# Kernel optimization log

Measured on AMD Instinct MI355X. Metric: run time of the kernel, lower is better.

Reference implementation:

```python
import jax, jax.numpy as jnp
import numpy as np

N_NODES = 50000
N_EDGES = 1000000
D_IN_V = 64
D_IN_A = 64
D_OUT_V = 64
D_OUT_A = 64


def setup_inputs() -> dict:
    key = jax.random.key(0)
    ks = jax.random.split(key, 12)
    s = 1.0 / np.sqrt(D_IN_V)
    sa = 1.0 / np.sqrt(D_IN_A)
    return {
        "x_v": jax.random.normal(ks[0], (N_NODES, D_IN_V), jnp.float32),
        "x_a": jax.random.normal(ks[1], (N_EDGES, D_IN_A), jnp.float32),
        "arc_index": jax.random.randint(ks[2], (2, N_EDGES), 0, N_NODES, jnp.int32),
        # torch.nn.Linear convention: weight [out, in], y = x @ W.T + b
        "W_vv": jax.random.uniform(ks[3], (D_OUT_V, D_IN_V), jnp.float32, -s, s),
        "b_vv": jax.random.uniform(ks[4], (D_OUT_V,), jnp.float32, -s, s),
        "W_va": jax.random.uniform(ks[5], (D_OUT_V, D_IN_A), jnp.float32, -sa, sa),
        "W_att": jax.random.uniform(ks[6], (1, D_IN_A), jnp.float32, -sa, sa),
        "b_att": jax.random.uniform(ks[7], (1,), jnp.float32, -sa, sa),
        "W_aa": jax.random.uniform(ks[8], (D_OUT_A, D_IN_A), jnp.float32, -sa, sa),
        "b_aa": jax.random.uniform(ks[9], (D_OUT_A,), jnp.float32, -sa, sa),
        "W_av": jax.random.uniform(ks[10], (D_OUT_A, D_IN_V), jnp.float32, -s, s),
    }


def reference(x_v, x_a, arc_index, W_vv, b_vv, W_va, W_att, b_att, W_aa, b_aa, W_av):
    src = arc_index[0]
    dst = arc_index[1]
    num_nodes = x_v.shape[0]

    # h_self = dense_vv(x_v)
    h_self = x_v @ W_vv.T + b_vv                      # [N, out_v]

    # per-edge attention logit e = attention_va(x_a).squeeze(-1)
    e = (x_a @ W_att.T + b_att)[:, 0]                 # [E]

    # segment softmax over incoming edges of each dst node (numerically stable)
    max_per_dst = jax.ops.segment_max(e, dst, num_segments=num_nodes)  # -inf for empty segments
    exp_e = jnp.exp(e - max_per_dst[dst])             # [E]
    denom = jax.ops.segment_sum(exp_e, dst, num_segments=num_nodes)
    attn = exp_e / denom[dst]                         # [E]

    # message = dense_va(x_a) * attn, scatter-add into dst
    msg = (x_a @ W_va.T) * attn[:, None]              # [E, out_v]
    h_msg = jax.ops.segment_sum(msg, dst, num_segments=num_nodes)
    h_v = h_msg + h_self

    # arc update: dense_aa(x_a) + dense_av(x_v[src]) + dense_av(x_v[dst])
    h_a = x_a @ W_aa.T + b_aa + x_v[src] @ W_av.T + x_v[dst] @ W_av.T
    return (h_v, h_a)
```

## Files before the change

### kernel.cpp

```cpp
#include <hip/hip_runtime.h>

#define NE 1000000
#define NN 50000
#define D 64

__global__ __launch_bounds__(256) void k_init(float4* __restrict__ acc4,
                                              float* __restrict__ denom){
  int i = blockIdx.x*256 + threadIdx.x;
  if (i < NN*D/4) acc4[i] = make_float4(0.f,0.f,0.f,0.f);
  if (i < NN)     denom[i] = 0.f;
}

__global__ __launch_bounds__(256) void k_node(const float* __restrict__ x_v,
    const float* __restrict__ W_vv, const float* __restrict__ b_vv,
    const float* __restrict__ W_av, float* __restrict__ h_v,
    float* __restrict__ p_av){
  __shared__ float4 xrow[4][2][16];
  int lane = threadIdx.x & 63;
  int wv   = threadIdx.x >> 6;
  int wid  = __builtin_amdgcn_readfirstlane(blockIdx.x*4 + wv);
  int nw   = gridDim.x*4;
  float4 wvv[16], wav[16];
  #pragma unroll
  for (int q = 0; q < 16; q++){
    wvv[q] = *(const float4*)(W_vv + lane*D + q*4);
    wav[q] = *(const float4*)(W_av + lane*D + q*4);
  }
  float bv = b_vv[lane];
  int p = 0;
  for (int n = wid; n < NN; n += nw, p ^= 1){
    float xv = x_v[(size_t)n*D + lane];
    ((float*)xrow[wv][p])[lane] = xv;
    float a0=0.f,a1=0.f,b0=0.f,b1=0.f;
    #pragma unroll
    for (int q = 0; q < 16; q++){
      float4 x4 = xrow[wv][p][q];
      a0 += x4.x*wvv[q].x; a1 += x4.y*wvv[q].y;
      a0 += x4.z*wvv[q].z; a1 += x4.w*wvv[q].w;
      b0 += x4.x*wav[q].x; b1 += x4.y*wav[q].y;
      b0 += x4.z*wav[q].z; b1 += x4.w*wav[q].w;
    }
    h_v[(size_t)n*D + lane]  = a0+a1+bv;
    p_av[(size_t)n*D + lane] = b0+b1;
  }
}

__global__ __launch_bounds__(256) void k_edge(const float* __restrict__ x_a,
    const int* __restrict__ src, const int* __restrict__ dst,
    const float* __restrict__ W_aa, const float* __restrict__ b_aa,
    const float* __restrict__ W_att, const float* __restrict__ b_att,
    const float* __restrict__ p_av, float* __restrict__ h_a,
    float* __restrict__ acc_y, float* __restrict__ denom){
  __shared__ float4 xrow[4][2][16];
  int lane = threadIdx.x & 63;
  int wv   = threadIdx.x >> 6;
  int wid  = __builtin_amdgcn_readfirstlane(blockIdx.x*4 + wv);
  int nw   = gridDim.x*4;
  float4 waa[16];
  #pragma unroll
  for (int q = 0; q < 16; q++)
    waa[q] = *(const float4*)(W_aa + lane*D + q*4);
  float ba   = b_aa[lane];
  float wt   = W_att[lane];
  float batt = b_att[0];
  int p = 0;
  for (int e = wid; e < NE; e += nw, p ^= 1){
    int s  = src[e];
    int d2 = dst[e];
    float xv = x_a[(size_t)e*D + lane];
    float ps = p_av[(size_t)s*D  + lane];
    float pd = p_av[(size_t)d2*D + lane];
    ((float*)xrow[wv][p])[lane] = xv;
    float el = xv*wt;
    #pragma unroll
    for (int m = 32; m >= 1; m >>= 1) el += __shfl_xor(el, m, 64);
    float w = __expf(el + batt);
    float a0=0.f,a1=0.f,a2=0.f,a3=0.f;
    #pragma unroll
    for (int q = 0; q < 16; q++){
      float4 x4 = xrow[wv][p][q];
      a0 += x4.x*waa[q].x; a1 += x4.y*waa[q].y;
      a2 += x4.z*waa[q].z; a3 += x4.w*waa[q].w;
    }
    h_a[(size_t)e*D + lane] = a0+a1+a2+a3 + ba + ps + pd;
    unsafeAtomicAdd(&acc_y[(size_t)d2*D + lane], w*xv);
    if (lane == 0) unsafeAtomicAdd(&denom[d2], w);
  }
}

__global__ __launch_bounds__(256) void k_finish(const float* __restrict__ acc_y,
    const float* __restrict__ denom, const float* __restrict__ W_va,
    float* __restrict__ h_v){
  __shared__ float4 yrow[4][2][16];
  int lane = threadIdx.x & 63;
  int wv   = threadIdx.x >> 6;
  int wid  = __builtin_amdgcn_readfirstlane(blockIdx.x*4 + wv);
  int nw   = gridDim.x*4;
  float4 wva[16];
  #pragma unroll
  for (int q = 0; q < 16; q++)
    wva[q] = *(const float4*)(W_va + lane*D + q*4);
  int p = 0;
  for (int n = wid; n < NN; n += nw, p ^= 1){
    float dn  = denom[n];
    float inv = (dn > 0.f) ? 1.f/dn : 0.f;
    float yv  = acc_y[(size_t)n*D + lane] * inv;
    ((float*)yrow[wv][p])[lane] = yv;
    float a0=0.f,a1=0.f,a2=0.f,a3=0.f;
    #pragma unroll
    for (int q = 0; q < 16; q++){
      float4 y4 = yrow[wv][p][q];
      a0 += y4.x*wva[q].x; a1 += y4.y*wva[q].y;
      a2 += y4.z*wva[q].z; a3 += y4.w*wva[q].w;
    }
    h_v[(size_t)n*D + lane] += a0+a1+a2+a3;
  }
}

extern "C" void kernel_launch(void* const* d_in, const int* in_sizes, int n_in,
                              void* d_out, int out_size, void* d_ws, size_t ws_size,
                              hipStream_t stream){
  const float* x_v   = (const float*)d_in[0];
  const float* x_a   = (const float*)d_in[1];
  const int*   arc   = (const int*)  d_in[2];
  const float* W_vv  = (const float*)d_in[3];
  const float* b_vv  = (const float*)d_in[4];
  const float* W_va  = (const float*)d_in[5];
  const float* W_att = (const float*)d_in[6];
  const float* b_att = (const float*)d_in[7];
  const float* W_aa  = (const float*)d_in[8];
  const float* b_aa  = (const float*)d_in[9];
  const float* W_av  = (const float*)d_in[10];

  float* out = (float*)d_out;
  float* h_v = out;
  float* h_a = out + (size_t)NN*D;

  float* wsf   = (float*)d_ws;
  float* acc_y = wsf;
  float* denom = wsf + (size_t)NN*D;
  float* p_av  = wsf + (size_t)NN*D + NN;

  const int* srcp = arc;
  const int* dstp = arc + NE;

  hipLaunchKernelGGL(k_init,   dim3((NN*D/4 + 255)/256), dim3(256), 0, stream,
                     (float4*)acc_y, denom);
  hipLaunchKernelGGL(k_node,   dim3(768),  dim3(256), 0, stream,
                     x_v, W_vv, b_vv, W_av, h_v, p_av);
  hipLaunchKernelGGL(k_edge,   dim3(2048), dim3(256), 0, stream,
                     x_a, srcp, dstp, W_aa, b_aa, W_att, b_att, p_av, h_a,
                     acc_y, denom);
  hipLaunchKernelGGL(k_finish, dim3(768),  dim3(256), 0, stream,
                     acc_y, denom, W_va, h_v);
}
```

Baseline: 915.5 us.

## Process four rows per wave with float4 loads and fuse zero-init into node kernel

Each wavefront now handles four edges or nodes per iteration. It loads 256 contiguous floats as float4 per lane, so each register-held weight row is reused across four rows and per-row loop overhead is amortized. In the edge kernel the attention logit is reduced within 16-lane groups, and atomics use per-group destination indices. The separate init kernel is folded into k_node to save a launch, and the node and finish grids grow. Risks: more atomics per lane, since each lane now issues four scalar atomics to different addresses, and more LDS traffic per iteration.

New measurement: 1.309 ms. 1.43x slower.

```diff
diff --git a/kernel.cpp b/kernel.cpp
--- a/kernel.cpp
+++ b/kernel.cpp
@@ -3,19 +3,20 @@
 #define NE 1000000
 #define NN 50000
 #define D 64
-
-__global__ __launch_bounds__(256) void k_init(float4* __restrict__ acc4,
-                                              float* __restrict__ denom){
-  int i = blockIdx.x*256 + threadIdx.x;
-  if (i < NN*D/4) acc4[i] = make_float4(0.f,0.f,0.f,0.f);
-  if (i < NN)     denom[i] = 0.f;
-}
+#define NG (NE/4)
+#define NGN (NN/4)
 
 __global__ __launch_bounds__(256) void k_node(const float* __restrict__ x_v,
     const float* __restrict__ W_vv, const float* __restrict__ b_vv,
     const float* __restrict__ W_av, float* __restrict__ h_v,
-    float* __restrict__ p_av){
-  __shared__ float4 xrow[4][2][16];
+    float* __restrict__ p_av, float4* __restrict__ acc4,
+    float* __restrict__ denom){
+  __shared__ float4 xs[4][2][64];
+  int tid = blockIdx.x*256 + threadIdx.x;
+  int nt  = gridDim.x*256;
+  for (int i = tid; i < NN*D/4; i += nt) acc4[i] = make_float4(0.f,0.f,0.f,0.f);
+  for (int i = tid; i < NN;     i += nt) denom[i] = 0.f;
+
   int lane = threadIdx.x & 63;
   int wv   = threadIdx.x >> 6;
   int wid  = __builtin_amdgcn_readfirstlane(blockIdx.x*4 + wv);
@@ -28,20 +29,37 @@
   }
   float bv = b_vv[lane];
   int p = 0;
-  for (int n = wid; n < NN; n += nw, p ^= 1){
-    float xv = x_v[(size_t)n*D + lane];
-    ((float*)xrow[wv][p])[lane] = xv;
-    float a0=0.f,a1=0.f,b0=0.f,b1=0.f;
+  for (int g = wid; g < NGN; g += nw, p ^= 1){
+    int n0 = g*4;
+    float4 xv = *(const float4*)(x_v + (size_t)n0*D + lane*4);
+    xs[wv][p][lane] = xv;
+    __builtin_amdgcn_wave_barrier();
+    float A0=0.f,A1=0.f,A2=0.f,A3=0.f;
+    float B0=0.f,B1=0.f,B2=0.f,B3=0.f;
     #pragma unroll
     for (int q = 0; q < 16; q++){
-      float4 x4 = xrow[wv][p][q];
-      a0 += x4.x*wvv[q].x; a1 += x4.y*wvv[q].y;
-      a0 += x4.z*wvv[q].z; a1 += x4.w*wvv[q].w;
-      b0 += x4.x*wav[q].x; b1 += x4.y*wav[q].y;
-      b0 += x4.z*wav[q].z; b1 += x4.w*wav[q].w;
+      float4 x0 = xs[wv][p][q];
+      float4 x1 = xs[wv][p][16+q];
+      float4 x2 = xs[wv][p][32+q];
+      float4 x3 = xs[wv][p][48+q];
+      float4 wq = wvv[q], aq = wav[q];
+      A0 += x0.x*wq.x + x0.y*wq.y + x0.z*wq.z + x0.w*wq.w;
+      A1 += x1.x*wq.x + x1.y*wq.y + x1.z*wq.z + x1.w*wq.w;
+      A2 += x2.x*wq.x + x2.y*wq.y + x2.z*wq.z + x2.w*wq.w;
+      A3 += x3.x*wq.x + x3.y*wq.y + x3.z*wq.z + x3.w*wq.w;
+      B0 += x0.x*aq.x + x0.y*aq.y + x0.z*aq.z + x0.w*aq.w;
+      B1 += x1.x*aq.x + x1.y*aq.y + x1.z*aq.z + x1.w*aq.w;
+      B2 += x2.x*aq.x + x2.y*aq.y + x2.z*aq.z + x2.w*aq.w;
+      B3 += x3.x*aq.x + x3.y*aq.y + x3.z*aq.z + x3.w*aq.w;
     }
-    h_v[(size_t)n*D + lane]  = a0+a1+bv;
-    p_av[(size_t)n*D + lane] = b0+b1;
+    h_v [(size_t)(n0+0)*D + lane] = A0 + bv;
+    h_v [(size_t)(n0+1)*D + lane] = A1 + bv;
+    h_v [(size_t)(n0+2)*D + lane] = A2 + bv;
+    h_v [(size_t)(n0+3)*D + lane] = A3 + bv;
+    p_av[(size_t)(n0+0)*D + lane] = B0;
+    p_av[(size_t)(n0+1)*D + lane] = B1;
+    p_av[(size_t)(n0+2)*D + lane] = B2;
+    p_av[(size_t)(n0+3)*D + lane] = B3;
   }
 }
 
@@ -51,7 +69,7 @@
     const float* __restrict__ W_att, const float* __restrict__ b_att,
     const float* __restrict__ p_av, float* __restrict__ h_a,
     float* __restrict__ acc_y, float* __restrict__ denom){
-  __shared__ float4 xrow[4][2][16];
+  __shared__ float4 xs[4][2][64];
   int lane = threadIdx.x & 63;
   int wv   = threadIdx.x >> 6;
   int wid  = __builtin_amdgcn_readfirstlane(blockIdx.x*4 + wv);
@@ -60,38 +78,72 @@
   #pragma unroll
   for (int q = 0; q < 16; q++)
     waa[q] = *(const float4*)(W_aa + lane*D + q*4);
-  float ba   = b_aa[lane];
-  float wt   = W_att[lane];
-  float batt = b_att[0];
+  float  ba   = b_aa[lane];
+  float4 wt4  = *(const float4*)(W_att + (lane & 15)*4);
+  float  batt = b_att[0];
+  int r = lane >> 4;
+
   int p = 0;
-  for (int e = wid; e < NE; e += nw, p ^= 1){
-    int s  = src[e];
-    int d2 = dst[e];
-    float xv = x_a[(size_t)e*D + lane];
-    float ps = p_av[(size_t)s*D  + lane];
-    float pd = p_av[(size_t)d2*D + lane];
-    ((float*)xrow[wv][p])[lane] = xv;
-    float el = xv*wt;
-    #pragma unroll
-    for (int m = 32; m >= 1; m >>= 1) el += __shfl_xor(el, m, 64);
+  for (int g = wid; g < NG; g += nw, p ^= 1){
+    int e0 = g*4;
+    int4 sv = *(const int4*)(src + e0);
+    int4 dv = *(const int4*)(dst + e0);
+    int s0 = __builtin_amdgcn_readfirstlane(sv.x);
+    int s1 = __builtin_amdgcn_readfirstlane(sv.y);
+    int s2 = __builtin_amdgcn_readfirstlane(sv.z);
+    int s3 = __builtin_amdgcn_readfirstlane(sv.w);
+    int d0 = __builtin_amdgcn_readfirstlane(dv.x);
+    int d1 = __builtin_amdgcn_readfirstlane(dv.y);
+    int d2 = __builtin_amdgcn_readfirstlane(dv.z);
+    int d3 = __builtin_amdgcn_readfirstlane(dv.w);
+    float4 xv = *(const float4*)(x_a + (size_t)e0*D + lane*4);
+    float ps0 = p_av[(size_t)s0*D + lane];
+    float ps1 = p_av[(size_t)s1*D + lane];
+    float ps2 = p_av[(size_t)s2*D + lane];
+    float ps3 = p_av[(size_t)s3*D + lane];
+    float pd0 = p_av[(size_t)d0*D + lane];
+    float pd1 = p_av[(size_t)d1*D + lane];
+    float pd2 = p_av[(size_t)d2*D + lane];
+    float pd3 = p_av[(size_t)d3*D + lane];
+    xs[wv][p][lane] = xv;
+    __builtin_amdgcn_wave_barrier();
+    float el = xv.x*wt4.x + xv.y*wt4.y + xv.z*wt4.z + xv.w*wt4.w;
+    el += __shfl_xor(el, 1, 64);
+    el += __shfl_xor(el, 2, 64);
+    el += __shfl_xor(el, 4, 64);
+    el += __shfl_xor(el, 8, 64);
     float w = __expf(el + batt);
-    float a0=0.f,a1=0.f,a2=0.f,a3=0.f;
+    float A0=0.f,A1=0.f,A2=0.f,A3=0.f;
     #pragma unroll
     for (int q = 0; q < 16; q++){
-      float4 x4 = xrow[wv][p][q];
-      a0 += x4.x*waa[q].x; a1 += x4.y*waa[q].y;
-      a2 += x4.z*waa[q].z; a3 += x4.w*waa[q].w;
+      float4 x0 = xs[wv][p][q];
+      float4 x1 = xs[wv][p][16+q];
+      float4 x2 = xs[wv][p][32+q];
+      float4 x3 = xs[wv][p][48+q];
+      float4 wq = waa[q];
+      A0 += x0.x*wq.x + x0.y*wq.y + x0.z*wq.z + x0.w*wq.w;
+      A1 += x1.x*wq.x + x1.y*wq.y + x1.z*wq.z + x1.w*wq.w;
+      A2 += x2.x*wq.x + x2.y*wq.y + x2.z*wq.z + x2.w*wq.w;
+      A3 += x3.x*wq.x + x3.y*wq.y + x3.z*wq.z + x3.w*wq.w;
     }
-    h_a[(size_t)e*D + lane] = a0+a1+a2+a3 + ba + ps + pd;
-    unsafeAtomicAdd(&acc_y[(size_t)d2*D + lane], w*xv);
-    if (lane == 0) unsafeAtomicAdd(&denom[d2], w);
+    h_a[(size_t)(e0+0)*D + lane] = A0 + ba + ps0 + pd0;
+    h_a[(size_t)(e0+1)*D + lane] = A1 + ba + ps1 + pd1;
+    h_a[(size_t)(e0+2)*D + lane] = A2 + ba + ps2 + pd2;
+    h_a[(size_t)(e0+3)*D + lane] = A3 + ba + ps3 + pd3;
+    int dsel = (r == 0) ? d0 : (r == 1) ? d1 : (r == 2) ? d2 : d3;
+    float* ap = acc_y + (size_t)dsel*D + (lane & 15)*4;
+    unsafeAtomicAdd(ap+0, w*xv.x);
+    unsafeAtomicAdd(ap+1, w*xv.y);
+    unsafeAtomicAdd(ap+2, w*xv.z);
+    unsafeAtomicAdd(ap+3, w*xv.w);
+    if ((lane & 15) == 0) unsafeAtomicAdd(&denom[dsel], w);
   }
 }
 
 __global__ __launch_bounds__(256) void k_finish(const float* __restrict__ acc_y,
     const float* __restrict__ denom, const float* __restrict__ W_va,
     float* __restrict__ h_v){
-  __shared__ float4 yrow[4][2][16];
+  __shared__ float4 ys[4][2][64];
   int lane = threadIdx.x & 63;
   int wv   = threadIdx.x >> 6;
   int wid  = __builtin_amdgcn_readfirstlane(blockIdx.x*4 + wv);
@@ -100,20 +152,34 @@
   #pragma unroll
   for (int q = 0; q < 16; q++)
     wva[q] = *(const float4*)(W_va + lane*D + q*4);
+  int r = lane >> 4;
   int p = 0;
-  for (int n = wid; n < NN; n += nw, p ^= 1){
-    float dn  = denom[n];
-    float inv = (dn > 0.f) ? 1.f/dn : 0.f;
-    float yv  = acc_y[(size_t)n*D + lane] * inv;
-    ((float*)yrow[wv][p])[lane] = yv;
-    float a0=0.f,a1=0.f,a2=0.f,a3=0.f;
+  for (int g = wid; g < NGN; g += nw, p ^= 1){
+    int n0 = g*4;
+    float4 dn = *(const float4*)(denom + n0);
+    float4 yv = *(const float4*)(acc_y + (size_t)n0*D + lane*4);
+    float dsel = (r == 0) ? dn.x : (r == 1) ? dn.y : (r == 2) ? dn.z : dn.w;
+    float inv  = (dsel > 0.f) ? 1.f/dsel : 0.f;
+    yv.x *= inv; yv.y *= inv; yv.z *= inv; yv.w *= inv;
+    ys[wv][p][lane] = yv;
+    __builtin_amdgcn_wave_barrier();
+    float A0=0.f,A1=0.f,A2=0.f,A3=0.f;
     #pragma unroll
     for (int q = 0; q < 16; q++){
-      float4 y4 = yrow[wv][p][q];
-      a0 += y4.x*wva[q].x; a1 += y4.y*wva[q].y;
-      a2 += y4.z*wva[q].z; a3 += y4.w*wva[q].w;
+      float4 y0 = ys[wv][p][q];
+      float4 y1 = ys[wv][p][16+q];
+      float4 y2 = ys[wv][p][32+q];
+      float4 y3 = ys[wv][p][48+q];
+      float4 wq = wva[q];
+      A0 += y0.x*wq.x + y0.y*wq.y + y0.z*wq.z + y0.w*wq.w;
+      A1 += y1.x*wq.x + y1.y*wq.y + y1.z*wq.z + y1.w*wq.w;
+      A2 += y2.x*wq.x + y2.y*wq.y + y2.z*wq.z + y2.w*wq.w;
+      A3 += y3.x*wq.x + y3.y*wq.y + y3.z*wq.z + y3.w*wq.w;
     }
-    h_v[(size_t)n*D + lane] += a0+a1+a2+a3;
+    h_v[(size_t)(n0+0)*D + lane] += A0;
+    h_v[(size_t)(n0+1)*D + lane] += A1;
+    h_v[(size_t)(n0+2)*D + lane] += A2;
+    h_v[(size_t)(n0+3)*D + lane] += A3;
   }
 }
 
@@ -144,13 +210,11 @@
   const int* srcp = arc;
   const int* dstp = arc + NE;
 
-  hipLaunchKernelGGL(k_init,   dim3((NN*D/4 + 255)/256), dim3(256), 0, stream,
-                     (float4*)acc_y, denom);
-  hipLaunchKernelGGL(k_node,   dim3(768),  dim3(256), 0, stream,
-                     x_v, W_vv, b_vv, W_av, h_v, p_av);
+  hipLaunchKernelGGL(k_node,   dim3(1024), dim3(256), 0, stream,
+                     x_v, W_vv, b_vv, W_av, h_v, p_av, (float4*)acc_y, denom);
   hipLaunchKernelGGL(k_edge,   dim3(2048), dim3(256), 0, stream,
                      x_a, srcp, dstp, W_aa, b_aa, W_att, b_att, p_av, h_a,
                      acc_y, denom);
-  hipLaunchKernelGGL(k_finish, dim3(768),  dim3(256), 0, stream,
+  hipLaunchKernelGGL(k_finish, dim3(1024), dim3(256), 0, stream,
                      acc_y, denom, W_va, h_v);
 }
```
